# Kernel optimization log

Hardware: AMD Instinct MI355X
Metric: run time of the kernel (lower is better)

The kernel has to match this reference:

```python
import jax, jax.numpy as jnp
import numpy as np

N = 50000      # nodes
E = 800000     # edges (avg degree 16)
D_IN, D_H, D_OUT = 128, 256, 128


def setup_inputs() -> dict:
    key = jax.random.key(0)
    ks = jax.random.split(key, 8)
    x = jax.random.normal(ks[0], (N, D_IN), dtype=jnp.float32)
    edge_index = jax.random.randint(ks[1], (2, E), 0, N, dtype=jnp.int64)
    s1 = 1.0 / np.sqrt(D_IN).astype(np.float32)
    s2 = 1.0 / np.sqrt(D_H).astype(np.float32)
    return {
        "x": x,
        "edge_index": edge_index,
        "W1l": jax.random.normal(ks[2], (D_H, D_IN), jnp.float32) * s1,
        "b1l": jnp.zeros((D_H,), jnp.float32),
        "W1r": jax.random.normal(ks[3], (D_H, D_IN), jnp.float32) * s1,
        "W2l": jax.random.normal(ks[4], (D_OUT, D_H), jnp.float32) * s2,
        "b2l": jnp.zeros((D_OUT,), jnp.float32),
        "W2r": jax.random.normal(ks[5], (D_OUT, D_H), jnp.float32) * s2,
    }


def sage_conv(x, src, dst, Wl, bl, Wr):
    # mean-aggregate source features into destination nodes
    agg = jax.ops.segment_sum(x[src], dst, num_segments=N)           # [N, d_in]
    deg = jax.ops.segment_sum(jnp.ones((src.shape[0],), x.dtype), dst, num_segments=N)
    mean = agg / jnp.maximum(deg, 1.0)[:, None]
    # lin_l(mean_agg) + lin_r(x_root); lin_r has no bias (PyG SAGEConv default)
    return mean @ Wl.T + bl + x @ Wr.T


def reference(x, edge_index, W1l, b1l, W1r, W2l, b2l, W2r):
    src, dst = edge_index[0], edge_index[1]
    h = sage_conv(x, src, dst, W1l, b1l, W1r)
    h = jax.nn.relu(h)  # dropout inactive in eval mode
    return sage_conv(h, src, dst, W2l, b2l, W2r)
```

## Files before the change

### kernel.cpp

```cpp
#include <hip/hip_runtime.h>


typedef __attribute__((ext_vector_type(8))) short bf16x8;
typedef __attribute__((ext_vector_type(4))) float floatx4;

__device__ inline unsigned short f2b(float f) {
  unsigned int x = __float_as_uint(f);
  unsigned int r = (x + 0x7fffu + ((x >> 16) & 1u)) >> 16;
  return (unsigned short)r;
}
__device__ inline float blo(unsigned int u) { return __uint_as_float(u << 16); }
__device__ inline float bhi(unsigned int u) { return __uint_as_float(u & 0xffff0000u); }

__global__ void prep_kernel(const float* __restrict__ x,
                            const float* __restrict__ W1l, const float* __restrict__ W1r,
                            const float* __restrict__ W2l, const float* __restrict__ W2r,
                            unsigned short* __restrict__ Wc1, unsigned short* __restrict__ Wc2,
                            unsigned short* __restrict__ A1,
                            int* __restrict__ cnt, int* __restrict__ off, int N, int E) {
  int i = blockIdx.x * blockDim.x + threadIdx.x;
  if (i < 65536) {
    int j = i >> 8, k = i & 255;
    float v1 = (k < 128) ? W1l[j * 128 + k] : W1r[j * 128 + (k - 128)];
    Wc1[i] = f2b(v1);
    float v2 = (j < 128) ? W2l[j * 256 + k] : W2r[(j - 128) * 256 + k];
    Wc2[i] = f2b(v2);
  }
  if (i < N) cnt[i] = 0;
  if (i == 0) off[N] = E;
  if (i < N * 32) {
    int n = i >> 5, c = (i & 31) * 4;
    float4 v = *(const float4*)(x + (size_t)n * 128 + c);
    uint2 p;
    p.x = (unsigned int)f2b(v.x) | ((unsigned int)f2b(v.y) << 16);
    p.y = (unsigned int)f2b(v.z) | ((unsigned int)f2b(v.w) << 16);
    *(uint2*)(A1 + (size_t)n * 256 + 128 + c) = p;
  }
}

__global__ void hist_kernel(const int* __restrict__ dst, int* __restrict__ cnt, int E) {
  int e = blockIdx.x * blockDim.x + threadIdx.x;
  if (e < E) atomicAdd(&cnt[dst[e]], 1);
}

__global__ __launch_bounds__(1024) void scan_blocks_kernel(const int* __restrict__ cnt,
                                                           int* __restrict__ off,
                                                           int* __restrict__ bsum, int N) {
  __shared__ int wsum[16];
  __shared__ int wincl[16];
  const int tid = threadIdx.x;
  const int lane = tid & 63;
  const int wv = tid >> 6;
  const int i = blockIdx.x * 1024 + tid;
  const int v = (i < N) ? cnt[i] : 0;
  int s = v;
#pragma unroll
  for (int o = 1; o < 64; o <<= 1) {
    int t = __shfl_up(s, o, 64);
    if (lane >= o) s += t;
  }
  if (lane == 63) wsum[wv] = s;
  __syncthreads();
  if (tid < 16) {
    int ws = wsum[tid];
#pragma unroll
    for (int o = 1; o < 16; o <<= 1) {
      int t = __shfl_up(ws, o, 16);
      if ((tid & 15) >= o) ws += t;
    }
    wincl[tid] = ws;
  }
  __syncthreads();
  const int wo = wv ? wincl[wv - 1] : 0;
  if (i < N) off[i] = wo + s - v;
  if (tid == 1023) bsum[blockIdx.x] = wo + s;
}

__global__ __launch_bounds__(1024) void scan_add_kernel(int* __restrict__ off, int* __restrict__ cur,
                                                        const int* __restrict__ bsum, int N, int SB) {
  __shared__ int bofs[64];
  const int tid = threadIdx.x;
  if (tid < 64) {
    int v = (tid < SB) ? bsum[tid] : 0;
    int s = v;
#pragma unroll
    for (int o = 1; o < 64; o <<= 1) {
      int t = __shfl_up(s, o, 64);
      if (tid >= o) s += t;
    }
    bofs[tid] = s - v;
  }
  __syncthreads();
  int i = blockIdx.x * 1024 + tid;
  if (i < N) {
    int o = off[i] + bofs[blockIdx.x];
    off[i] = o;
    cur[i] = o;
  }
}

__global__ void fill_kernel(const int* __restrict__ src, const int* __restrict__ dst,
                            int* __restrict__ cur, int* __restrict__ csr, int E, int chunks) {
  int pass = blockIdx.x / chunks;
  int c = blockIdx.x - pass * chunks;
  int e = c * 256 + threadIdx.x;
  if (e >= E) return;
  int d = dst[e];
  if ((d >> 14) != pass) return;
  int p = atomicAdd(&cur[d], 1);
  csr[p] = src[e];
}

__global__ void gather1_kernel(const unsigned short* __restrict__ feat,
                               const int* __restrict__ csr, const int* __restrict__ off,
                               unsigned short* __restrict__ ob, int N) {
  int wid = (blockIdx.x * blockDim.x + threadIdx.x) >> 6;
  if (wid >= N) return;
  const int lane = threadIdx.x & 63;
  const int sub = lane >> 4;
  const int col8 = (lane & 15) * 8;
  const int s0 = off[wid], s1 = off[wid + 1];
  float a[8] = {};
  int e = s0 + sub;
  for (; e + 4 < s1; e += 8) {
    int i0 = csr[e], i1 = csr[e + 4];
    uint4 u = *(const uint4*)(feat + (size_t)i0 * 256 + col8);
    uint4 w = *(const uint4*)(feat + (size_t)i1 * 256 + col8);
    a[0] += blo(u.x); a[1] += bhi(u.x); a[2] += blo(u.y); a[3] += bhi(u.y);
    a[4] += blo(u.z); a[5] += bhi(u.z); a[6] += blo(u.w); a[7] += bhi(u.w);
    a[0] += blo(w.x); a[1] += bhi(w.x); a[2] += blo(w.y); a[3] += bhi(w.y);
    a[4] += blo(w.z); a[5] += bhi(w.z); a[6] += blo(w.w); a[7] += bhi(w.w);
  }
  if (e < s1) {
    int i0 = csr[e];
    uint4 u = *(const uint4*)(feat + (size_t)i0 * 256 + col8);
    a[0] += blo(u.x); a[1] += bhi(u.x); a[2] += blo(u.y); a[3] += bhi(u.y);
    a[4] += blo(u.z); a[5] += bhi(u.z); a[6] += blo(u.w); a[7] += bhi(u.w);
  }
#pragma unroll
  for (int k = 0; k < 8; k++) {
    a[k] += __shfl_xor(a[k], 16, 64);
    a[k] += __shfl_xor(a[k], 32, 64);
  }
  if (sub == 0) {
    const float inv = 1.0f / fmaxf((float)(s1 - s0), 1.0f);
    uint4 p;
    p.x = (unsigned int)f2b(a[0] * inv) | ((unsigned int)f2b(a[1] * inv) << 16);
    p.y = (unsigned int)f2b(a[2] * inv) | ((unsigned int)f2b(a[3] * inv) << 16);
    p.z = (unsigned int)f2b(a[4] * inv) | ((unsigned int)f2b(a[5] * inv) << 16);
    p.w = (unsigned int)f2b(a[6] * inv) | ((unsigned int)f2b(a[7] * inv) << 16);
    *(uint4*)(ob + (size_t)wid * 256 + col8) = p;
  }
}

__global__ void gather2_kernel(const unsigned short* __restrict__ t,
                               const int* __restrict__ csr, const int* __restrict__ off,
                               float* __restrict__ out, int N) {
  int wid = (blockIdx.x * blockDim.x + threadIdx.x) >> 6;
  if (wid >= N) return;
  const int lane = threadIdx.x & 63;
  const int sub = lane >> 4;
  const int col8 = (lane & 15) * 8;
  const int s0 = off[wid], s1 = off[wid + 1];
  float a[8] = {};
  int e = s0 + sub;
  for (; e + 4 < s1; e += 8) {
    int i0 = csr[e], i1 = csr[e + 4];
    uint4 u = *(const uint4*)(t + (size_t)i0 * 128 + col8);
    uint4 w = *(const uint4*)(t + (size_t)i1 * 128 + col8);
    a[0] += blo(u.x); a[1] += bhi(u.x); a[2] += blo(u.y); a[3] += bhi(u.y);
    a[4] += blo(u.z); a[5] += bhi(u.z); a[6] += blo(u.w); a[7] += bhi(u.w);
    a[0] += blo(w.x); a[1] += bhi(w.x); a[2] += blo(w.y); a[3] += bhi(w.y);
    a[4] += blo(w.z); a[5] += bhi(w.z); a[6] += blo(w.w); a[7] += bhi(w.w);
  }
  if (e < s1) {
    int i0 = csr[e];
    uint4 u = *(const uint4*)(t + (size_t)i0 * 128 + col8);
    a[0] += blo(u.x); a[1] += bhi(u.x); a[2] += blo(u.y); a[3] += bhi(u.y);
    a[4] += blo(u.z); a[5] += bhi(u.z); a[6] += blo(u.w); a[7] += bhi(u.w);
  }
#pragma unroll
  for (int k = 0; k < 8; k++) {
    a[k] += __shfl_xor(a[k], 16, 64);
    a[k] += __shfl_xor(a[k], 32, 64);
  }
  if (sub == 0) {
    const float inv = 1.0f / fmaxf((float)(s1 - s0), 1.0f);
    float4* o = (float4*)(out + (size_t)wid * 128 + col8);
    float4 c0 = o[0], c1 = o[1];
    c0.x += a[0] * inv; c0.y += a[1] * inv; c0.z += a[2] * inv; c0.w += a[3] * inv;
    c1.x += a[4] * inv; c1.y += a[5] * inv; c1.z += a[6] * inv; c1.w += a[7] * inv;
    o[0] = c0; o[1] = c1;
  }
}

template <int MODE>
__global__ __launch_bounds__(256, 2)
void gemm_bf16(const unsigned short* __restrict__ A, const unsigned short* __restrict__ W,
               const float* __restrict__ bias, unsigned short* __restrict__ Hout,
               float* __restrict__ Fout, int M) {
  constexpr int LDA = 72;
  __shared__ __align__(16) unsigned short As[128 * LDA];
  __shared__ __align__(16) unsigned short Ws[128 * LDA];
  const int t = threadIdx.x;
  const int lane = t & 63;
  const int wave = t >> 6;
  const int wm = (wave & 1) * 64;
  const int wn = (wave >> 1) * 64;
  const int l15 = lane & 15;
  const int quad = lane >> 4;
  const int m_blk = blockIdx.x * 128;
  const int j_blk = blockIdx.y * 128;

  floatx4 acc[4][4] = {};

  for (int kc = 0; kc < 256; kc += 64) {
    __syncthreads();
#pragma unroll
    for (int i = 0; i < 4; i++) {
      int c = t + 256 * i;
      int row = c >> 3;
      int col = (c & 7) * 8;
      int ar = m_blk + row;
      if (ar >= M) ar = M - 1;
      uint4 av = *(const uint4*)(A + (size_t)ar * 256 + kc + col);
      *(uint4*)(As + row * LDA + col) = av;
      uint4 wv = *(const uint4*)(W + (size_t)(j_blk + row) * 256 + kc + col);
      *(uint4*)(Ws + row * LDA + col) = wv;
    }
    __syncthreads();
#pragma unroll
    for (int ks = 0; ks < 64; ks += 32) {
      bf16x8 af[4], bfr[4];
#pragma unroll
      for (int mt = 0; mt < 4; mt++)
        af[mt] = *(const bf16x8*)(As + (wm + mt * 16 + l15) * LDA + ks + quad * 8);
#pragma unroll
      for (int nt = 0; nt < 4; nt++)
        bfr[nt] = *(const bf16x8*)(Ws + (wn + nt * 16 + l15) * LDA + ks + quad * 8);
#pragma unroll
      for (int mt = 0; mt < 4; mt++)
#pragma unroll
        for (int nt = 0; nt < 4; nt++)
          acc[mt][nt] = __builtin_amdgcn_mfma_f32_16x16x32_bf16(af[mt], bfr[nt], acc[mt][nt], 0, 0, 0);
    }
  }

#pragma unroll
  for (int mt = 0; mt < 4; mt++) {
#pragma unroll
    for (int nt = 0; nt < 4; nt++) {
      const int jl = wn + nt * 16 + l15;
      float bv = 0.f;
      if (MODE == 0) bv = bias[j_blk + jl];
      else if (j_blk != 0) bv = bias[jl];
#pragma unroll
      for (int r = 0; r < 4; r++) {
        const int node = m_blk + wm + mt * 16 + quad * 4 + r;
        if (node >= M) continue;
        const float v = acc[mt][nt][r];
        if (MODE == 0) {
          Hout[(size_t)node * 256 + j_blk + jl] = f2b(fmaxf(v + bv, 0.f));
        } else if (j_blk == 0) {
          Hout[(size_t)node * 128 + jl] = f2b(v);
        } else {
          Fout[(size_t)node * 128 + jl] = v + bv;
        }
      }
    }
  }
}

extern "C" void kernel_launch(void* const* d_in, const int* in_sizes, int n_in,
                              void* d_out, int out_size, void* d_ws, size_t ws_size,
                              hipStream_t stream) {
  const float* x   = (const float*)d_in[0];
  const int*  eidx = (const int*)d_in[1];
  const float* W1l = (const float*)d_in[2];
  const float* b1l = (const float*)d_in[3];
  const float* W1r = (const float*)d_in[4];
  const float* W2l = (const float*)d_in[5];
  const float* b2l = (const float*)d_in[6];
  const float* W2r = (const float*)d_in[7];
  float* out = (float*)d_out;

  const int N = in_sizes[0] / 128;
  const int E = in_sizes[1] / 2;
  const int* src = eidx;
  const int* dst = eidx + E;

  int* cnt  = (int*)d_ws;
  int* off  = cnt + N;
  int* bsum = off + N + 1;
  int* csr  = bsum + 64;
  size_t ioff = ((size_t)(N + N + 1 + 64 + E) * 4 + 15) & ~(size_t)15;
  unsigned short* A1  = (unsigned short*)((char*)d_ws + ioff);
  unsigned short* h   = A1 + (size_t)N * 256;
  unsigned short* tb  = h + (size_t)N * 256;
  unsigned short* Wc1 = tb + (size_t)N * 128;
  unsigned short* Wc2 = Wc1 + 65536;

  const int SB = (N + 1023) / 1024;

  prep_kernel<<<(N * 32 + 255) / 256, 256, 0, stream>>>(x, W1l, W1r, W2l, W2r,
                                                        Wc1, Wc2, A1, cnt, off, N, E);
  hist_kernel<<<(E + 255) / 256, 256, 0, stream>>>(dst, cnt, E);
  scan_blocks_kernel<<<SB, 1024, 0, stream>>>(cnt, off, bsum, N);
  scan_add_kernel<<<SB, 1024, 0, stream>>>(off, cnt, bsum, N, SB);

  const int chunks = (E + 255) / 256;
  fill_kernel<<<chunks * 4, 256, 0, stream>>>(src, dst, cnt, csr, E, chunks);

  const int gblocks = (N + 3) / 4;
  gather1_kernel<<<gblocks, 256, 0, stream>>>(A1 + 128, csr, off, A1, N);

  dim3 gg((N + 127) / 128, 2);
  gemm_bf16<0><<<gg, 256, 0, stream>>>(A1, Wc1, b1l, h, nullptr, N);
  gemm_bf16<1><<<gg, 256, 0, stream>>>(h, Wc2, b2l, tb, out, N);
  gather2_kernel<<<gblocks, 256, 0, stream>>>(tb, csr, off, out, N);
}
```

Baseline: 301.0 us.

## Record per-edge ranks in histogram to build CSR without fill atomics; widen gather slots

The histogram kernel now keeps the atomicAdd return value as a per-edge rank. The fill kernel then writes each edge to csr[off[dst]+rank] with no atomics and in a single pass, replacing the four-pass atomic fill. Both kernels process four edges per thread using int4 loads. The gather kernels now use 8 edge slots of 8 lanes each, with every lane loading two 16-byte chunks per row, which puts more independent row loads in flight at the cost of more registers and a longer shuffle reduction.

```diff
diff --git a/kernel.cpp b/kernel.cpp
--- a/kernel.cpp
+++ b/kernel.cpp
@@ -11,6 +11,14 @@
 }
 __device__ inline float blo(unsigned int u) { return __uint_as_float(u << 16); }
 __device__ inline float bhi(unsigned int u) { return __uint_as_float(u & 0xffff0000u); }
+
+#define ACC8(A, u)                                            \
+  {                                                           \
+    A[0] += blo((u).x); A[1] += bhi((u).x);                   \
+    A[2] += blo((u).y); A[3] += bhi((u).y);                   \
+    A[4] += blo((u).z); A[5] += bhi((u).z);                   \
+    A[6] += blo((u).w); A[7] += bhi((u).w);                   \
+  }
 
 __global__ void prep_kernel(const float* __restrict__ x,
                             const float* __restrict__ W1l, const float* __restrict__ W1r,
@@ -38,9 +46,21 @@
   }
 }
 
-__global__ void hist_kernel(const int* __restrict__ dst, int* __restrict__ cnt, int E) {
-  int e = blockIdx.x * blockDim.x + threadIdx.x;
-  if (e < E) atomicAdd(&cnt[dst[e]], 1);
+__global__ void hist_kernel(const int* __restrict__ dst, int* __restrict__ cnt,
+                            int* __restrict__ rank, int E) {
+  int i = blockIdx.x * blockDim.x + threadIdx.x;
+  int e = i * 4;
+  if (e + 3 < E) {
+    int4 d = *(const int4*)(dst + e);
+    int4 r;
+    r.x = atomicAdd(&cnt[d.x], 1);
+    r.y = atomicAdd(&cnt[d.y], 1);
+    r.z = atomicAdd(&cnt[d.z], 1);
+    r.w = atomicAdd(&cnt[d.w], 1);
+    *(int4*)(rank + e) = r;
+  } else {
+    for (; e < E; e++) rank[e] = atomicAdd(&cnt[dst[e]], 1);
+  }
 }
 
 __global__ __launch_bounds__(1024) void scan_blocks_kernel(const int* __restrict__ cnt,
@@ -76,7 +96,7 @@
   if (tid == 1023) bsum[blockIdx.x] = wo + s;
 }
 
-__global__ __launch_bounds__(1024) void scan_add_kernel(int* __restrict__ off, int* __restrict__ cur,
+__global__ __launch_bounds__(1024) void scan_add_kernel(int* __restrict__ off,
                                                         const int* __restrict__ bsum, int N, int SB) {
   __shared__ int bofs[64];
   const int tid = threadIdx.x;
@@ -92,23 +112,25 @@
   }
   __syncthreads();
   int i = blockIdx.x * 1024 + tid;
-  if (i < N) {
-    int o = off[i] + bofs[blockIdx.x];
-    off[i] = o;
-    cur[i] = o;
-  }
+  if (i < N) off[i] = off[i] + bofs[blockIdx.x];
 }
 
 __global__ void fill_kernel(const int* __restrict__ src, const int* __restrict__ dst,
-                            int* __restrict__ cur, int* __restrict__ csr, int E, int chunks) {
-  int pass = blockIdx.x / chunks;
-  int c = blockIdx.x - pass * chunks;
-  int e = c * 256 + threadIdx.x;
-  if (e >= E) return;
-  int d = dst[e];
-  if ((d >> 14) != pass) return;
-  int p = atomicAdd(&cur[d], 1);
-  csr[p] = src[e];
+                            const int* __restrict__ rank, const int* __restrict__ off,
+                            int* __restrict__ csr, int E) {
+  int i = blockIdx.x * blockDim.x + threadIdx.x;
+  int e = i * 4;
+  if (e + 3 < E) {
+    int4 d = *(const int4*)(dst + e);
+    int4 r = *(const int4*)(rank + e);
+    int4 s = *(const int4*)(src + e);
+    csr[off[d.x] + r.x] = s.x;
+    csr[off[d.y] + r.y] = s.y;
+    csr[off[d.z] + r.z] = s.z;
+    csr[off[d.w] + r.w] = s.w;
+  } else {
+    for (; e < E; e++) csr[off[dst[e]] + rank[e]] = src[e];
+  }
 }
 
 __global__ void gather1_kernel(const unsigned short* __restrict__ feat,
@@ -117,39 +139,46 @@
   int wid = (blockIdx.x * blockDim.x + threadIdx.x) >> 6;
   if (wid >= N) return;
   const int lane = threadIdx.x & 63;
-  const int sub = lane >> 4;
-  const int col8 = (lane & 15) * 8;
+  const int slot = lane >> 3;
+  const int j = lane & 7;
+  const int c0 = j * 8;
   const int s0 = off[wid], s1 = off[wid + 1];
-  float a[8] = {};
-  int e = s0 + sub;
-  for (; e + 4 < s1; e += 8) {
-    int i0 = csr[e], i1 = csr[e + 4];
-    uint4 u = *(const uint4*)(feat + (size_t)i0 * 256 + col8);
-    uint4 w = *(const uint4*)(feat + (size_t)i1 * 256 + col8);
-    a[0] += blo(u.x); a[1] += bhi(u.x); a[2] += blo(u.y); a[3] += bhi(u.y);
-    a[4] += blo(u.z); a[5] += bhi(u.z); a[6] += blo(u.w); a[7] += bhi(u.w);
-    a[0] += blo(w.x); a[1] += bhi(w.x); a[2] += blo(w.y); a[3] += bhi(w.y);
-    a[4] += blo(w.z); a[5] += bhi(w.z); a[6] += blo(w.w); a[7] += bhi(w.w);
-  }
-  if (e < s1) {
+  float a[16] = {};
+  int e = s0 + slot;
+  for (; e + 8 < s1; e += 16) {
+    int i0 = csr[e], i1 = csr[e + 8];
+    uint4 u0 = *(const uint4*)(feat + (size_t)i0 * 256 + c0);
+    uint4 v0 = *(const uint4*)(feat + (size_t)i0 * 256 + 64 + c0);
+    uint4 u1 = *(const uint4*)(feat + (size_t)i1 * 256 + c0);
+    uint4 v1 = *(const uint4*)(feat + (size_t)i1 * 256 + 64 + c0);
+    ACC8(a, u0); ACC8((a + 8), v0);
+    ACC8(a, u1); ACC8((a + 8), v1);
+  }
+  for (; e < s1; e += 8) {
     int i0 = csr[e];
-    uint4 u = *(const uint4*)(feat + (size_t)i0 * 256 + col8);
-    a[0] += blo(u.x); a[1] += bhi(u.x); a[2] += blo(u.y); a[3] += bhi(u.y);
-    a[4] += blo(u.z); a[5] += bhi(u.z); a[6] += blo(u.w); a[7] += bhi(u.w);
-  }
-#pragma unroll
-  for (int k = 0; k < 8; k++) {
+    uint4 u0 = *(const uint4*)(feat + (size_t)i0 * 256 + c0);
+    uint4 v0 = *(const uint4*)(feat + (size_t)i0 * 256 + 64 + c0);
+    ACC8(a, u0); ACC8((a + 8), v0);
+  }
+#pragma unroll
+  for (int k = 0; k < 16; k++) {
+    a[k] += __shfl_xor(a[k], 8, 64);
     a[k] += __shfl_xor(a[k], 16, 64);
     a[k] += __shfl_xor(a[k], 32, 64);
   }
-  if (sub == 0) {
+  if (slot == 0) {
     const float inv = 1.0f / fmaxf((float)(s1 - s0), 1.0f);
     uint4 p;
     p.x = (unsigned int)f2b(a[0] * inv) | ((unsigned int)f2b(a[1] * inv) << 16);
     p.y = (unsigned int)f2b(a[2] * inv) | ((unsigned int)f2b(a[3] * inv) << 16);
     p.z = (unsigned int)f2b(a[4] * inv) | ((unsigned int)f2b(a[5] * inv) << 16);
     p.w = (unsigned int)f2b(a[6] * inv) | ((unsigned int)f2b(a[7] * inv) << 16);
-    *(uint4*)(ob + (size_t)wid * 256 + col8) = p;
+    *(uint4*)(ob + (size_t)wid * 256 + c0) = p;
+    p.x = (unsigned int)f2b(a[8] * inv) | ((unsigned int)f2b(a[9] * inv) << 16);
+    p.y = (unsigned int)f2b(a[10] * inv) | ((unsigned int)f2b(a[11] * inv) << 16);
+    p.z = (unsigned int)f2b(a[12] * inv) | ((unsigned int)f2b(a[13] * inv) << 16);
+    p.w = (unsigned int)f2b(a[14] * inv) | ((unsigned int)f2b(a[15] * inv) << 16);
+    *(uint4*)(ob + (size_t)wid * 256 + 64 + c0) = p;
   }
 }
 
@@ -159,38 +188,43 @@
   int wid = (blockIdx.x * blockDim.x + threadIdx.x) >> 6;
   if (wid >= N) return;
   const int lane = threadIdx.x & 63;
-  const int sub = lane >> 4;
-  const int col8 = (lane & 15) * 8;
+  const int slot = lane >> 3;
+  const int j = lane & 7;
+  const int c0 = j * 8;
   const int s0 = off[wid], s1 = off[wid + 1];
-  float a[8] = {};
-  int e = s0 + sub;
-  for (; e + 4 < s1; e += 8) {
-    int i0 = csr[e], i1 = csr[e + 4];
-    uint4 u = *(const uint4*)(t + (size_t)i0 * 128 + col8);
-    uint4 w = *(const uint4*)(t + (size_t)i1 * 128 + col8);
-    a[0] += blo(u.x); a[1] += bhi(u.x); a[2] += blo(u.y); a[3] += bhi(u.y);
-    a[4] += blo(u.z); a[5] += bhi(u.z); a[6] += blo(u.w); a[7] += bhi(u.w);
-    a[0] += blo(w.x); a[1] += bhi(w.x); a[2] += blo(w.y); a[3] += bhi(w.y);
-    a[4] += blo(w.z); a[5] += bhi(w.z); a[6] += blo(w.w); a[7] += bhi(w.w);
-  }
-  if (e < s1) {
+  float a[16] = {};
+  int e = s0 + slot;
+  for (; e + 8 < s1; e += 16) {
+    int i0 = csr[e], i1 = csr[e + 8];
+    uint4 u0 = *(const uint4*)(t + (size_t)i0 * 128 + c0);
+    uint4 v0 = *(const uint4*)(t + (size_t)i0 * 128 + 64 + c0);
+    uint4 u1 = *(const uint4*)(t + (size_t)i1 * 128 + c0);
+    uint4 v1 = *(const uint4*)(t + (size_t)i1 * 128 + 64 + c0);
+    ACC8(a, u0); ACC8((a + 8), v0);
+    ACC8(a, u1); ACC8((a + 8), v1);
+  }
+  for (; e < s1; e += 8) {
     int i0 = csr[e];
-    uint4 u = *(const uint4*)(t + (size_t)i0 * 128 + col8);
-    a[0] += blo(u.x); a[1] += bhi(u.x); a[2] += blo(u.y); a[3] += bhi(u.y);
-    a[4] += blo(u.z); a[5] += bhi(u.z); a[6] += blo(u.w); a[7] += bhi(u.w);
-  }
-#pragma unroll
-  for (int k = 0; k < 8; k++) {
+    uint4 u0 = *(const uint4*)(t + (size_t)i0 * 128 + c0);
+    uint4 v0 = *(const uint4*)(t + (size_t)i0 * 128 + 64 + c0);
+    ACC8(a, u0); ACC8((a + 8), v0);
+  }
+#pragma unroll
+  for (int k = 0; k < 16; k++) {
+    a[k] += __shfl_xor(a[k], 8, 64);
     a[k] += __shfl_xor(a[k], 16, 64);
     a[k] += __shfl_xor(a[k], 32, 64);
   }
-  if (sub == 0) {
+  if (slot == 0) {
     const float inv = 1.0f / fmaxf((float)(s1 - s0), 1.0f);
-    float4* o = (float4*)(out + (size_t)wid * 128 + col8);
-    float4 c0 = o[0], c1 = o[1];
-    c0.x += a[0] * inv; c0.y += a[1] * inv; c0.z += a[2] * inv; c0.w += a[3] * inv;
-    c1.x += a[4] * inv; c1.y += a[5] * inv; c1.z += a[6] * inv; c1.w += a[7] * inv;
-    o[0] = c0; o[1] = c1;
+    float4* o0 = (float4*)(out + (size_t)wid * 128 + c0);
+    float4* o1 = (float4*)(out + (size_t)wid * 128 + 64 + c0);
+    float4 r0 = o0[0], r1 = o0[1], r2 = o1[0], r3 = o1[1];
+    r0.x += a[0] * inv;  r0.y += a[1] * inv;  r0.z += a[2] * inv;  r0.w += a[3] * inv;
+    r1.x += a[4] * inv;  r1.y += a[5] * inv;  r1.z += a[6] * inv;  r1.w += a[7] * inv;
+    r2.x += a[8] * inv;  r2.y += a[9] * inv;  r2.z += a[10] * inv; r2.w += a[11] * inv;
+    r3.x += a[12] * inv; r3.y += a[13] * inv; r3.z += a[14] * inv; r3.w += a[15] * inv;
+    o0[0] = r0; o0[1] = r1; o1[0] = r2; o1[1] = r3;
   }
 }
 
@@ -292,8 +326,9 @@
   int* cnt  = (int*)d_ws;
   int* off  = cnt + N;
   int* bsum = off + N + 1;
-  int* csr  = bsum + 64;
-  size_t ioff = ((size_t)(N + N + 1 + 64 + E) * 4 + 15) & ~(size_t)15;
+  int* rank = bsum + 64;
+  int* csr  = rank + E;
+  size_t ioff = ((size_t)(N + N + 1 + 64 + 2 * E) * 4 + 15) & ~(size_t)15;
   unsigned short* A1  = (unsigned short*)((char*)d_ws + ioff);
   unsigned short* h   = A1 + (size_t)N * 256;
   unsigned short* tb  = h + (size_t)N * 256;
@@ -304,12 +339,10 @@
 
   prep_kernel<<<(N * 32 + 255) / 256, 256, 0, stream>>>(x, W1l, W1r, W2l, W2r,
                                                         Wc1, Wc2, A1, cnt, off, N, E);
-  hist_kernel<<<(E + 255) / 256, 256, 0, stream>>>(dst, cnt, E);
+  hist_kernel<<<(E / 4 + 255) / 256, 256, 0, stream>>>(dst, cnt, rank, E);
   scan_blocks_kernel<<<SB, 1024, 0, stream>>>(cnt, off, bsum, N);
-  scan_add_kernel<<<SB, 1024, 0, stream>>>(off, cnt, bsum, N, SB);
-
-  const int chunks = (E + 255) / 256;
-  fill_kernel<<<chunks * 4, 256, 0, stream>>>(src, dst, cnt, csr, E, chunks);
+  scan_add_kernel<<<SB, 1024, 0, stream>>>(off, bsum, N, SB);
+  fill_kernel<<<(E / 4 + 255) / 256, 256, 0, stream>>>(src, dst, rank, off, csr, E);
 
   const int gblocks = (N + 3) / 4;
   gather1_kernel<<<gblocks, 256, 0, stream>>>(A1 + 128, csr, off, A1, N);
```

Result: faster. 274.1 us (-8.9%).
